# Performance work log

Hardware: AMD Instinct MI355X
Metric: run time of the kernel (lower is better)

Reference implementation:

```python
import jax, jax.numpy as jnp
import numpy as np

N = 50000      # nodes
E = 400000     # edges per hop
IN = 256       # in_channels
H = 4          # heads
C = 64         # out_channels per head
NEG = 0.2      # leaky relu negative slope


def setup_inputs() -> dict:
    key = jax.random.key(0)
    ks = jax.random.split(key, 10)
    x = jax.random.normal(ks[0], (N, IN), dtype=jnp.float32)
    edge_index1 = jax.random.randint(ks[1], (2, E), 0, N, dtype=jnp.int32)
    edge_index2 = jax.random.randint(ks[2], (2, E), 0, N, dtype=jnp.int32)
    s = 0.05
    Wl0 = jax.random.normal(ks[3], (IN, H * C), dtype=jnp.float32) * s
    Wr0 = jax.random.normal(ks[4], (IN, H * C), dtype=jnp.float32) * s
    att0 = jax.random.normal(ks[5], (H, C), dtype=jnp.float32) * s
    Wl1 = jax.random.normal(ks[6], (IN, H * C), dtype=jnp.float32) * s
    Wr1 = jax.random.normal(ks[7], (IN, H * C), dtype=jnp.float32) * s
    att1 = jax.random.normal(ks[8], (H, C), dtype=jnp.float32) * s
    return {"x": x, "Wl0": Wl0, "Wr0": Wr0, "att0": att0,
            "Wl1": Wl1, "Wr1": Wr1, "att1": att1,
            "edge_index1": edge_index1, "edge_index2": edge_index2}


def _gatv2_hop(x, Wl, Wr, att, src, dst):
    """One GATv2Conv hop (bias=False, residual=False, eval-mode dropout, concat=False)."""
    n = x.shape[0]
    xl = (x @ Wl).reshape(n, H, C)   # source-side projection
    xr = (x @ Wr).reshape(n, H, C)   # target-side projection
    # edge-wise GATv2 score: a^T leaky_relu(x_l[j] + x_r[i])
    m = jax.nn.leaky_relu(xl[src] + xr[dst], NEG)            # [E, H, C]
    e = jnp.einsum('ehc,hc->eh', m, att)                     # [E, H]
    # segment softmax over incoming edges of each destination node
    e_max = jax.lax.stop_gradient(
        jax.ops.segment_max(e, dst, num_segments=n))         # [N, H]
    ex = jnp.exp(e - e_max[dst])
    denom = jax.ops.segment_sum(ex, dst, num_segments=n)     # [N, H]
    alpha = ex / (denom[dst] + 1e-16)                        # [E, H]
    msg = xl[src] * alpha[:, :, None]                        # [E, H, C]
    out = jax.ops.segment_sum(msg, dst, num_segments=n)      # [N, H, C]
    return out.mean(axis=1)                                  # concat=False -> mean heads


def reference(x, Wl0, Wr0, att0, Wl1, Wr1, att1, edge_index1, edge_index2):
    n = x.shape[0]
    # hop 0: add_self_loops=True
    loop = jnp.arange(n, dtype=edge_index1.dtype)
    src0 = jnp.concatenate([edge_index1[0], loop])
    dst0 = jnp.concatenate([edge_index1[1], loop])
    out = _gatv2_hop(x, Wl0, Wr0, att0, src0, dst0)
    # hop 1: no self loops, scaled by 1/(k+1) = 1/2
    out = out + _gatv2_hop(x, Wl1, Wr1, att1, edge_index2[0], edge_index2[1]) / 2.0
    return out
```

## Files before the change

kernel.cpp:

```cpp
#include <hip/hip_runtime.h>

typedef unsigned int uint;
typedef unsigned short ushort;

typedef __bf16 bf16x8 __attribute__((ext_vector_type(8)));
typedef float f32x4 __attribute__((ext_vector_type(4)));
typedef float f32x2 __attribute__((ext_vector_type(2)));

#define CAP 48
#define RSTR 136

__device__ __forceinline__ ushort f2bf(float f) {
    uint u = __float_as_uint(f);
    u += 0x7fffu + ((u >> 16) & 1u);
    return (ushort)(u >> 16);
}
__device__ __forceinline__ void load_lds16(const ushort* g, ushort* l) {
    __builtin_amdgcn_global_load_lds(
        (const __attribute__((address_space(1))) void*)g,
        (__attribute__((address_space(3))) void*)l, 16, 0, 0);
}
__device__ __forceinline__ f32x2 up2(uint u) {
    f32x2 r;
    r.x = __uint_as_float(u << 16);
    r.y = __uint_as_float(u & 0xffff0000u);
    return r;
}

template<int CTRL>
__device__ __forceinline__ float dppadd(float p) {
    int t = __builtin_amdgcn_update_dpp(0, __float_as_int(p), CTRL, 0xf, 0xf, true);
    return p + __int_as_float(t);
}

__global__ __launch_bounds__(256) void prep_scatter(
    const float* __restrict__ X, ushort* __restrict__ Xb, int Nrows, int Mpad,
    const float* __restrict__ Wl0, const float* __restrict__ Wr0,
    const float* __restrict__ Wl1, const float* __restrict__ Wr1,
    ushort* __restrict__ Wt,
    const int* __restrict__ ei1, const int* __restrict__ ei2,
    int* __restrict__ cnt0, int* __restrict__ srcs0,
    int* __restrict__ cnt1, int* __restrict__ srcs1,
    int E1, int E2, int SB)
{
    int blk = blockIdx.x;
    if (blk < SB) {
        int e = blk * 256 + threadIdx.x;
        if (e < E1) {
            int d = ei1[E1 + e];
            int pos = atomicAdd(&cnt0[d], 1);
            if (pos < CAP) srcs0[(size_t)d * CAP + pos] = ei1[e];
        } else if (e < E1 + E2) {
            int e2 = e - E1;
            int d = ei2[E2 + e2];
            int pos = atomicAdd(&cnt1[d], 1);
            if (pos < CAP) srcs1[(size_t)d * CAP + pos] = ei2[e2];
        }
        return;
    }
    blk -= SB;
    const int BX = Mpad / 8;
    if (blk < BX) {
        int i = blk * 256 + threadIdx.x;
        int base = i * 8;
        int row = base >> 8;
        ushort o[8];
        if (row < Nrows) {
            float4 v0 = *(const float4*)(X + base);
            float4 v1 = *(const float4*)(X + base + 4);
            o[0] = f2bf(v0.x); o[1] = f2bf(v0.y); o[2] = f2bf(v0.z); o[3] = f2bf(v0.w);
            o[4] = f2bf(v1.x); o[5] = f2bf(v1.y); o[6] = f2bf(v1.z); o[7] = f2bf(v1.w);
        } else {
#pragma unroll
            for (int j = 0; j < 8; j++) o[j] = 0;
        }
        *(uint4*)(Xb + base) = *(const uint4*)o;
        return;
    }
    blk -= BX;
    int n = blk;
    int k = threadIdx.x;
    const float* W = (n < 256) ? Wl0 : (n < 512) ? Wr0 : (n < 768) ? Wl1 : Wr1;
    Wt[n * 256 + k] = f2bf(W[k * 256 + (n & 255)]);
}

__global__ __launch_bounds__(256, 2) void gemm_mfma(
    const ushort* __restrict__ Xb,
    const ushort* __restrict__ Wt,
    ushort* __restrict__ XP,
    int Nrows, int Pp, int nbshift)
{
    int b = blockIdx.x;
    int xcd = b & 7;
    int i = b >> 3;
    int p = xcd * Pp + (i >> nbshift);
    int j = i & ((1 << nbshift) - 1);
    const int m0 = p * 128;
    const int n0g = j * 128;

    __shared__ ushort SH[4 * 128 * 64];

    const int tid = threadIdx.x;
    const int w = tid >> 6, l = tid & 63;
    const int wm = w & 1, wn = w >> 1;

    f32x4 acc[4][4];
#pragma unroll
    for (int ii = 0; ii < 4; ii++)
#pragma unroll
        for (int jj = 0; jj < 4; jj++) acc[ii][jj] = (f32x4)(0.f);

    const int fr = l & 15, fq = l >> 4;
    int a_off[2][4], b_off[2][4];
#pragma unroll
    for (int g = 0; g < 2; g++)
#pragma unroll
        for (int t = 0; t < 4; t++) {
            int c = g * 4 + fq;
            int rA = wm * 64 + t * 16 + fr;
            a_off[g][t] = (rA * 8 + ((c + rA) & 7)) * 8;
            int rB = wn * 64 + t * 16 + fr;
            b_off[g][t] = (rB * 8 + ((c + rB) & 7)) * 8;
        }

    int srow[4], schunk[4];
#pragma unroll
    for (int rnd = 0; rnd < 4; rnd++) {
        int slot = rnd * 256 + tid;
        srow[rnd] = slot >> 3;
        schunk[rnd] = ((slot & 7) - srow[rnd]) & 7;
    }

#pragma unroll
    for (int rnd = 0; rnd < 4; rnd++) {
        load_lds16(Xb + (size_t)(m0 + srow[rnd]) * 256 + schunk[rnd] * 8,
                   &SH[(rnd * 256 + w * 64) * 8]);
        load_lds16(Wt + (size_t)(n0g + srow[rnd]) * 256 + schunk[rnd] * 8,
                   &SH[8192 + (rnd * 256 + w * 64) * 8]);
    }
    __syncthreads();

    int cur = 0;
    for (int t = 0; t < 4; t++) {
        const ushort* As = SH + cur * 16384;
        const ushort* Bs = As + 8192;
        if (t < 3) {
            ushort* An = SH + (cur ^ 1) * 16384;
            ushort* Bn = An + 8192;
            const int k0n = (t + 1) * 64;
#pragma unroll
            for (int rnd = 0; rnd < 4; rnd++) {
                load_lds16(Xb + (size_t)(m0 + srow[rnd]) * 256 + k0n + schunk[rnd] * 8,
                           &An[(rnd * 256 + w * 64) * 8]);
                load_lds16(Wt + (size_t)(n0g + srow[rnd]) * 256 + k0n + schunk[rnd] * 8,
                           &Bn[(rnd * 256 + w * 64) * 8]);
            }
        }
#pragma unroll
        for (int g = 0; g < 2; g++) {
            bf16x8 a[4], bfr[4];
#pragma unroll
            for (int t4 = 0; t4 < 4; t4++) {
                a[t4]   = *(const bf16x8*)(As + a_off[g][t4]);
                bfr[t4] = *(const bf16x8*)(Bs + b_off[g][t4]);
            }
#pragma unroll
            for (int mi = 0; mi < 4; mi++)
#pragma unroll
                for (int ni = 0; ni < 4; ni++)
                    acc[mi][ni] = __builtin_amdgcn_mfma_f32_16x16x32_bf16(
                        a[mi], bfr[ni], acc[mi][ni], 0, 0, 0);
        }
        __syncthreads();
        cur ^= 1;
    }

    ushort* OUT = XP + (size_t)(n0g >> 8) * ((size_t)Nrows * 256);
    const int colbase = n0g & 255;
    const int cb = wn * 64 + fr;
#pragma unroll
    for (int r = 0; r < 2; r++) {
        __syncthreads();
#pragma unroll
        for (int mm = 0; mm < 2; mm++) {
            int mi = 2 * r + mm;
            int brb = (wm * 32 + mm * 16 + fq * 4) * RSTR + cb;
#pragma unroll
            for (int reg = 0; reg < 4; reg++)
#pragma unroll
                for (int ni = 0; ni < 4; ni++)
                    SH[brb + reg * RSTR + ni * 16] = f2bf(acc[mi][ni][reg]);
        }
        __syncthreads();
        int br = tid >> 2;
        int grow = m0 + (br >> 5) * 64 + (2 * r + ((br >> 4) & 1)) * 16 + (br & 15);
        bool ok = (grow < Nrows);
        int cc = (tid & 3) * 8;
#pragma unroll
        for (int q = 0; q < 4; q++) {
            uint4 v = *(const uint4*)(SH + br * RSTR + cc + q * 32);
            if (ok) *(uint4*)(OUT + (size_t)grow * 256 + colbase + cc + q * 32) = v;
        }
    }
}

__device__ __forceinline__ uint4 pair_load(const ushort* __restrict__ XL, int sv,
                                           int e, int cp, uint hl, uint sub16)
{
    int eA = (e     < cp) ? e     : cp;
    int eB = (e + 1 < cp) ? e + 1 : cp;
    uint sA = (uint)__builtin_amdgcn_readlane(sv, eA) * 512u;
    uint sB = (uint)__builtin_amdgcn_readlane(sv, eB) * 512u;
    uint off = sA + hl * (sB - sA) + sub16;
    return *(const uint4*)((const char*)XL + off);
}

__device__ __forceinline__ void eaccp(uint4 raw, int deadB, uint hl,
    const f32x2* __restrict__ xr2, const f32x2* __restrict__ av2,
    f32x2* __restrict__ acc, float& den)
{
    f32x2 xv[4];
    xv[0] = up2(raw.x);
    xv[1] = up2(raw.y);
    xv[2] = up2(raw.z);
    xv[3] = up2(raw.w);
    f32x2 p2 = (f32x2)(0.f);
#pragma unroll
    for (int k = 0; k < 4; k++) {
        f32x2 t = xv[k] + xr2[k];
        f32x2 u = t * 0.2f;
        t = __builtin_elementwise_max(t, u);
        p2 += t * av2[k];
    }
    float p = p2.x + p2.y;
    p = dppadd<0xB1>(p);
    p = dppadd<0x4E>(p);
    p = dppadd<0x141>(p);
    float pe = __expf(p);
    if (deadB & (int)hl) pe = 0.f;
    den += pe;
#pragma unroll
    for (int k = 0; k < 4; k++) acc[k] += xv[k] * pe;
}

__device__ __forceinline__ void gat_hop_core(
    const ushort* __restrict__ XL, const float* __restrict__ att,
    int mt, int sv, uint4 xrr, uint hl, uint sub, uint sub16,
    f32x2* __restrict__ acc, float& den)
{
#pragma unroll
    for (int k = 0; k < 4; k++) acc[k] = (f32x2)(0.f);
    den = 0.f;
    if (mt <= 0) return;

    f32x2 xr2[4];
    xr2[0] = up2(xrr.x);
    xr2[1] = up2(xrr.y);
    xr2[2] = up2(xrr.z);
    xr2[3] = up2(xrr.w);
    float4 a0 = *(const float4*)(att + sub * 8);
    float4 a1 = *(const float4*)(att + sub * 8 + 4);
    f32x2 av2[4];
    av2[0].x = a0.x; av2[0].y = a0.y;
    av2[1].x = a0.z; av2[1].y = a0.w;
    av2[2].x = a1.x; av2[2].y = a1.y;
    av2[3].x = a1.z; av2[3].y = a1.w;

    const int cp = mt - 1;
    uint4 pf0 = pair_load(XL, sv, 0, cp, hl, sub16);
    uint4 pf1 = pair_load(XL, sv, 2, cp, hl, sub16);
    uint4 pf2 = pair_load(XL, sv, 4, cp, hl, sub16);
    for (int i = 0; i < mt; i += 6) {
        uint4 c0 = pf0, c1 = pf1, c2 = pf2;
        pf0 = pair_load(XL, sv, i + 6,  cp, hl, sub16);
        pf1 = pair_load(XL, sv, i + 8,  cp, hl, sub16);
        pf2 = pair_load(XL, sv, i + 10, cp, hl, sub16);
        eaccp(c0, (i + 1 >= mt) ? 1 : 0, hl, xr2, av2, acc, den);
        if (i + 2 < mt)
            eaccp(c1, (i + 3 >= mt) ? 1 : 0, hl, xr2, av2, acc, den);
        if (i + 4 < mt)
            eaccp(c2, (i + 5 >= mt) ? 1 : 0, hl, xr2, av2, acc, den);
    }
}

__global__ __launch_bounds__(256) void gat_fused(
    const ushort* __restrict__ XL0, const ushort* __restrict__ XR0,
    const float* __restrict__ att0,
    const int* __restrict__ cnt0, const int* __restrict__ srcs0,
    int self0, float scale0,
    const ushort* __restrict__ XL1, const ushort* __restrict__ XR1,
    const float* __restrict__ att1,
    const int* __restrict__ cnt1, const int* __restrict__ srcs1,
    float scale1,
    const float* __restrict__ base, float* __restrict__ outp, int N)
{
    int d = blockIdx.x * 4 + (threadIdx.x >> 6);
    if (d >= N) return;
    int lane = threadIdx.x & 63;
    uint hl = (uint)(lane >> 5);
    uint sub = (uint)(lane & 31);
    uint sub16 = sub * 16u;

    int idx0 = lane - self0;
    idx0 = idx0 < 0 ? 0 : (idx0 > CAP - 1 ? CAP - 1 : idx0);
    int sv0 = srcs0[(size_t)d * CAP + idx0];
    int m0 = __builtin_amdgcn_readfirstlane(cnt0[d]);
    uint4 xrr0 = *(const uint4*)((const char*)XR0 + (uint)d * 512u + sub16);

    int sv1 = 0, m1 = 0;
    uint4 xrr1 = {0, 0, 0, 0};
    if (cnt1) {
        int idx1 = lane > CAP - 1 ? CAP - 1 : lane;
        sv1 = srcs1[(size_t)d * CAP + idx1];
        m1 = __builtin_amdgcn_readfirstlane(cnt1[d]);
        xrr1 = *(const uint4*)((const char*)XR1 + (uint)d * 512u + sub16);
    }

    if (m0 > CAP) m0 = CAP;
    const int mt0 = m0 + self0;
    if (self0 && lane == 0) sv0 = d;
    if (m1 > CAP) m1 = CAP;

    f32x2 acc0[4];
    float den0;
    gat_hop_core(XL0, att0, mt0, sv0, xrr0, hl, sub, sub16, acc0, den0);

    float v[8];
    den0 += __shfl_xor(den0, 32);
    float s0 = scale0 / (den0 + 1e-16f);
    if (cnt1) {
        f32x2 acc1[4];
        float den1;
        gat_hop_core(XL1, att1, m1, sv1, xrr1, hl, sub, sub16, acc1, den1);
        den1 += __shfl_xor(den1, 32);
        float s1 = scale1 / (den1 + 1e-16f);
#pragma unroll
        for (int k = 0; k < 4; k++) {
            v[2 * k]     = acc0[k].x * s0 + acc1[k].x * s1;
            v[2 * k + 1] = acc0[k].y * s0 + acc1[k].y * s1;
        }
    } else {
#pragma unroll
        for (int k = 0; k < 4; k++) {
            v[2 * k]     = acc0[k].x * s0;
            v[2 * k + 1] = acc0[k].y * s0;
        }
    }
#pragma unroll
    for (int j = 0; j < 8; j++) {
        v[j] += __shfl_xor(v[j], 8);
        v[j] += __shfl_xor(v[j], 16);
        v[j] += __shfl_xor(v[j], 32);
    }
    if (lane < 8) {
        float* dst = outp + (size_t)d * 64 + lane * 8;
        float4 w0 = {v[0], v[1], v[2], v[3]};
        float4 w1 = {v[4], v[5], v[6], v[7]};
        if (base) {
            float4 b0 = *(const float4*)(base + (size_t)d * 64 + lane * 8);
            float4 b1 = *(const float4*)(base + (size_t)d * 64 + lane * 8 + 4);
            w0.x += b0.x; w0.y += b0.y; w0.z += b0.z; w0.w += b0.w;
            w1.x += b1.x; w1.y += b1.y; w1.z += b1.z; w1.w += b1.w;
        }
        *(float4*)dst = w0;
        *(float4*)(dst + 4) = w1;
    }
}

extern "C" void kernel_launch(void* const* d_in, const int* in_sizes, int n_in,
                              void* d_out, int out_size, void* d_ws, size_t ws_size,
                              hipStream_t stream)
{
    const float* x    = (const float*)d_in[0];
    const float* Wl0  = (const float*)d_in[1];
    const float* Wr0  = (const float*)d_in[2];
    const float* att0 = (const float*)d_in[3];
    const float* Wl1  = (const float*)d_in[4];
    const float* Wr1  = (const float*)d_in[5];
    const float* att1 = (const float*)d_in[6];
    const int* ei1 = (const int*)d_in[7];
    const int* ei2 = (const int*)d_in[8];

    const int N  = in_sizes[0] / 256;
    const int E1 = in_sizes[7] / 2;
    const int E2 = in_sizes[8] / 2;
    const int Mpad = ((N + 1023) / 1024) * 1024;
    const int P  = Mpad / 128;
    const int Pp = P / 8;
    const size_t NB = (size_t)N * 256;

    char* ws = (char*)d_ws;
    size_t off = 0;
    ushort* Xb  = (ushort*)(ws + off); off += (size_t)Mpad * 256 * sizeof(ushort);
    ushort* Wt  = (ushort*)(ws + off); off += (size_t)1024 * 256 * sizeof(ushort);
    int* cnt0   = (int*)(ws + off);    off += (size_t)N * sizeof(int);
    int* cnt1   = (int*)(ws + off);    off += (size_t)N * sizeof(int);
    int* srcs0  = (int*)(ws + off);    off += (size_t)N * CAP * sizeof(int);
    int* srcs1  = (int*)(ws + off);    off += (size_t)N * CAP * sizeof(int);
    ushort* XP  = (ushort*)(ws + off);
    size_t need_mega = off + 4 * NB * sizeof(ushort);
    const bool mega = (ws_size >= need_mega);
    float* outf = (float*)d_out;

    hipMemsetAsync(cnt0, 0, 2 * (size_t)N * sizeof(int), stream);

    const int BX = Mpad / 8;
    const int SB = (E1 + E2 + 255) / 256;
    prep_scatter<<<SB + BX + 1024, 256, 0, stream>>>(
        x, Xb, N, Mpad, Wl0, Wr0, Wl1, Wr1, Wt,
        ei1, ei2, cnt0, srcs0, cnt1, srcs1, E1, E2, SB);

    int aggblk = (N + 3) / 4;
    if (mega) {
        gemm_mfma<<<P * 8, 256, 0, stream>>>(Xb, Wt, XP, N, Pp, 3);
        gat_fused<<<aggblk, 256, 0, stream>>>(
            XP, XP + NB, att0, cnt0, srcs0, 1, 0.25f,
            XP + 2 * NB, XP + 3 * NB, att1, cnt1, srcs1, 0.125f,
            nullptr, outf, N);
    } else {
        gemm_mfma<<<P * 4, 256, 0, stream>>>(Xb, Wt, XP, N, Pp, 2);
        gat_fused<<<aggblk, 256, 0, stream>>>(
            XP, XP + NB, att0, cnt0, srcs0, 1, 0.25f,
            nullptr, nullptr, nullptr, nullptr, nullptr, 0.f,
            nullptr, outf, N);
        gemm_mfma<<<P * 4, 256, 0, stream>>>(Xb, Wt + 512 * 256, XP, N, Pp, 2);
        gat_fused<<<aggblk, 256, 0, stream>>>(
            XP, XP + NB, att1, cnt1, srcs1, 0, 0.125f,
            nullptr, nullptr, nullptr, nullptr, nullptr, 0.f,
            outf, outf, N);
    }
}
```

Before: 253.3 us.

## Issue all first-16-edge gathers for both hops upfront with inline asm loads

Replaces the per-hop software-pipelined gather loop with a single upfront burst of 16 global_load_dwordx4 per wave: 8 edge pairs for hop 0 and 8 for hop 1. Waits are placed with explicit vmcnt so hop-1 loads stay in flight while hop 0 is computed. Edges beyond 16 fall back to a simple serial loop. A launch_bounds occupancy hint of 4 is added. The aim is more memory-level parallelism on the random neighbor gathers, at the cost of many more live VGPRs. Edges past 16 lose prefetching.

```diff
diff --git a/kernel.cpp b/kernel.cpp
--- a/kernel.cpp
+++ b/kernel.cpp
@@ -6,6 +6,7 @@
 typedef __bf16 bf16x8 __attribute__((ext_vector_type(8)));
 typedef float f32x4 __attribute__((ext_vector_type(4)));
 typedef float f32x2 __attribute__((ext_vector_type(2)));
+typedef uint u32x4 __attribute__((ext_vector_type(4)));
 
 #define CAP 48
 #define RSTR 136
@@ -32,6 +33,10 @@
     int t = __builtin_amdgcn_update_dpp(0, __float_as_int(p), CTRL, 0xf, 0xf, true);
     return p + __int_as_float(t);
 }
+
+#define GLOAD(dst, voff, basep) \
+    asm volatile("global_load_dwordx4 %0, %1, %2" \
+                 : "=v"(dst) : "v"(voff), "s"(basep) : "memory")
 
 __global__ __launch_bounds__(256) void prep_scatter(
     const float* __restrict__ X, ushort* __restrict__ Xb, int Nrows, int Mpad,
@@ -204,26 +209,24 @@
     }
 }
 
-__device__ __forceinline__ uint4 pair_load(const ushort* __restrict__ XL, int sv,
-                                           int e, int cp, uint hl, uint sub16)
+__device__ __forceinline__ uint pair_voff(int sv, int e, int cp, uint hl, uint sub16)
 {
     int eA = (e     < cp) ? e     : cp;
     int eB = (e + 1 < cp) ? e + 1 : cp;
     uint sA = (uint)__builtin_amdgcn_readlane(sv, eA) * 512u;
     uint sB = (uint)__builtin_amdgcn_readlane(sv, eB) * 512u;
-    uint off = sA + hl * (sB - sA) + sub16;
-    return *(const uint4*)((const char*)XL + off);
-}
-
-__device__ __forceinline__ void eaccp(uint4 raw, int deadB, uint hl,
+    return (hl ? sB : sA) + sub16;
+}
+
+__device__ __forceinline__ void eaccp(u32x4 raw, int deadB, uint hl,
     const f32x2* __restrict__ xr2, const f32x2* __restrict__ av2,
     f32x2* __restrict__ acc, float& den)
 {
     f32x2 xv[4];
-    xv[0] = up2(raw.x);
-    xv[1] = up2(raw.y);
-    xv[2] = up2(raw.z);
-    xv[3] = up2(raw.w);
+    xv[0] = up2(raw[0]);
+    xv[1] = up2(raw[1]);
+    xv[2] = up2(raw[2]);
+    xv[3] = up2(raw[3]);
     f32x2 p2 = (f32x2)(0.f);
 #pragma unroll
     for (int k = 0; k < 4; k++) {
@@ -243,47 +246,7 @@
     for (int k = 0; k < 4; k++) acc[k] += xv[k] * pe;
 }
 
-__device__ __forceinline__ void gat_hop_core(
-    const ushort* __restrict__ XL, const float* __restrict__ att,
-    int mt, int sv, uint4 xrr, uint hl, uint sub, uint sub16,
-    f32x2* __restrict__ acc, float& den)
-{
-#pragma unroll
-    for (int k = 0; k < 4; k++) acc[k] = (f32x2)(0.f);
-    den = 0.f;
-    if (mt <= 0) return;
-
-    f32x2 xr2[4];
-    xr2[0] = up2(xrr.x);
-    xr2[1] = up2(xrr.y);
-    xr2[2] = up2(xrr.z);
-    xr2[3] = up2(xrr.w);
-    float4 a0 = *(const float4*)(att + sub * 8);
-    float4 a1 = *(const float4*)(att + sub * 8 + 4);
-    f32x2 av2[4];
-    av2[0].x = a0.x; av2[0].y = a0.y;
-    av2[1].x = a0.z; av2[1].y = a0.w;
-    av2[2].x = a1.x; av2[2].y = a1.y;
-    av2[3].x = a1.z; av2[3].y = a1.w;
-
-    const int cp = mt - 1;
-    uint4 pf0 = pair_load(XL, sv, 0, cp, hl, sub16);
-    uint4 pf1 = pair_load(XL, sv, 2, cp, hl, sub16);
-    uint4 pf2 = pair_load(XL, sv, 4, cp, hl, sub16);
-    for (int i = 0; i < mt; i += 6) {
-        uint4 c0 = pf0, c1 = pf1, c2 = pf2;
-        pf0 = pair_load(XL, sv, i + 6,  cp, hl, sub16);
-        pf1 = pair_load(XL, sv, i + 8,  cp, hl, sub16);
-        pf2 = pair_load(XL, sv, i + 10, cp, hl, sub16);
-        eaccp(c0, (i + 1 >= mt) ? 1 : 0, hl, xr2, av2, acc, den);
-        if (i + 2 < mt)
-            eaccp(c1, (i + 3 >= mt) ? 1 : 0, hl, xr2, av2, acc, den);
-        if (i + 4 < mt)
-            eaccp(c2, (i + 5 >= mt) ? 1 : 0, hl, xr2, av2, acc, den);
-    }
-}
-
-__global__ __launch_bounds__(256) void gat_fused(
+__global__ __launch_bounds__(256, 4) void gat_fused(
     const ushort* __restrict__ XL0, const ushort* __restrict__ XR0,
     const float* __restrict__ att0,
     const int* __restrict__ cnt0, const int* __restrict__ srcs0,
@@ -296,42 +259,110 @@
 {
     int d = blockIdx.x * 4 + (threadIdx.x >> 6);
     if (d >= N) return;
-    int lane = threadIdx.x & 63;
-    uint hl = (uint)(lane >> 5);
-    uint sub = (uint)(lane & 31);
-    uint sub16 = sub * 16u;
+    const int lane = threadIdx.x & 63;
+    const uint hl = (uint)(lane >> 5);
+    const uint sub = (uint)(lane & 31);
+    const uint sub16 = sub * 16u;
+    const bool two = (cnt1 != nullptr);
 
     int idx0 = lane - self0;
     idx0 = idx0 < 0 ? 0 : (idx0 > CAP - 1 ? CAP - 1 : idx0);
     int sv0 = srcs0[(size_t)d * CAP + idx0];
     int m0 = __builtin_amdgcn_readfirstlane(cnt0[d]);
-    uint4 xrr0 = *(const uint4*)((const char*)XR0 + (uint)d * 512u + sub16);
+    u32x4 xrr0 = *(const u32x4*)((const char*)XR0 + (uint)d * 512u + sub16);
+    float4 a00 = *(const float4*)(att0 + sub * 8);
+    float4 a01 = *(const float4*)(att0 + sub * 8 + 4);
 
     int sv1 = 0, m1 = 0;
-    uint4 xrr1 = {0, 0, 0, 0};
-    if (cnt1) {
+    u32x4 xrr1 = (u32x4)(0u);
+    float4 a10 = {0.f, 0.f, 0.f, 0.f}, a11 = {0.f, 0.f, 0.f, 0.f};
+    if (two) {
         int idx1 = lane > CAP - 1 ? CAP - 1 : lane;
         sv1 = srcs1[(size_t)d * CAP + idx1];
         m1 = __builtin_amdgcn_readfirstlane(cnt1[d]);
-        xrr1 = *(const uint4*)((const char*)XR1 + (uint)d * 512u + sub16);
+        xrr1 = *(const u32x4*)((const char*)XR1 + (uint)d * 512u + sub16);
+        a10 = *(const float4*)(att1 + sub * 8);
+        a11 = *(const float4*)(att1 + sub * 8 + 4);
     }
 
     if (m0 > CAP) m0 = CAP;
     const int mt0 = m0 + self0;
     if (self0 && lane == 0) sv0 = d;
+    if (mt0 == 0) sv0 = d;
     if (m1 > CAP) m1 = CAP;
+    const int mt1 = m1;
+    if (two && mt1 == 0) sv1 = d;
+
+    f32x2 xr20[4], av20[4], xr21[4], av21[4];
+    xr20[0] = up2(xrr0[0]); xr20[1] = up2(xrr0[1]);
+    xr20[2] = up2(xrr0[2]); xr20[3] = up2(xrr0[3]);
+    av20[0].x = a00.x; av20[0].y = a00.y;
+    av20[1].x = a00.z; av20[1].y = a00.w;
+    av20[2].x = a01.x; av20[2].y = a01.y;
+    av20[3].x = a01.z; av20[3].y = a01.w;
+    xr21[0] = up2(xrr1[0]); xr21[1] = up2(xrr1[1]);
+    xr21[2] = up2(xrr1[2]); xr21[3] = up2(xrr1[3]);
+    av21[0].x = a10.x; av21[0].y = a10.y;
+    av21[1].x = a10.z; av21[1].y = a10.w;
+    av21[2].x = a11.x; av21[2].y = a11.y;
+    av21[3].x = a11.z; av21[3].y = a11.w;
+
+    const int cp0 = mt0 > 0 ? mt0 - 1 : 0;
+    const int cp1 = mt1 > 0 ? mt1 - 1 : 0;
+    uint vo0[8], vo1[8];
+#pragma unroll
+    for (int k = 0; k < 8; k++) vo0[k] = pair_voff(sv0, 2 * k, cp0, hl, sub16);
+    if (two) {
+#pragma unroll
+        for (int k = 0; k < 8; k++) vo1[k] = pair_voff(sv1, 2 * k, cp1, hl, sub16);
+    }
+
+    __builtin_amdgcn_sched_barrier(0);
+    u32x4 p0[8], p1[8];
+#pragma unroll
+    for (int k = 0; k < 8; k++) GLOAD(p0[k], vo0[k], XL0);
+    if (two) {
+#pragma unroll
+        for (int k = 0; k < 8; k++) GLOAD(p1[k], vo1[k], XL1);
+        asm volatile("s_waitcnt vmcnt(8)" ::: "memory");
+    } else {
+        asm volatile("s_waitcnt vmcnt(0)" ::: "memory");
+    }
+    __builtin_amdgcn_sched_barrier(0);
 
     f32x2 acc0[4];
-    float den0;
-    gat_hop_core(XL0, att0, mt0, sv0, xrr0, hl, sub, sub16, acc0, den0);
-
-    float v[8];
+    float den0 = 0.f;
+#pragma unroll
+    for (int k = 0; k < 4; k++) acc0[k] = (f32x2)(0.f);
+#pragma unroll
+    for (int k = 0; k < 8; k++)
+        if (2 * k < mt0)
+            eaccp(p0[k], (2 * k + 1 >= mt0) ? 1 : 0, hl, xr20, av20, acc0, den0);
+    for (int i = 16; i < mt0; i += 2) {
+        uint vo = pair_voff(sv0, i, cp0, hl, sub16);
+        u32x4 c = *(const u32x4*)((const char*)XL0 + vo);
+        eaccp(c, (i + 1 >= mt0) ? 1 : 0, hl, xr20, av20, acc0, den0);
+    }
     den0 += __shfl_xor(den0, 32);
     float s0 = scale0 / (den0 + 1e-16f);
-    if (cnt1) {
+
+    float v[8];
+    if (two) {
+        asm volatile("s_waitcnt vmcnt(0)" ::: "memory");
+        __builtin_amdgcn_sched_barrier(0);
         f32x2 acc1[4];
-        float den1;
-        gat_hop_core(XL1, att1, m1, sv1, xrr1, hl, sub, sub16, acc1, den1);
+        float den1 = 0.f;
+#pragma unroll
+        for (int k = 0; k < 4; k++) acc1[k] = (f32x2)(0.f);
+#pragma unroll
+        for (int k = 0; k < 8; k++)
+            if (2 * k < mt1)
+                eaccp(p1[k], (2 * k + 1 >= mt1) ? 1 : 0, hl, xr21, av21, acc1, den1);
+        for (int i = 16; i < mt1; i += 2) {
+            uint vo = pair_voff(sv1, i, cp1, hl, sub16);
+            u32x4 c = *(const u32x4*)((const char*)XL1 + vo);
+            eaccp(c, (i + 1 >= mt1) ? 1 : 0, hl, xr21, av21, acc1, den1);
+        }
         den1 += __shfl_xor(den1, 32);
         float s1 = scale1 / (den1 + 1e-16f);
 #pragma unroll
```

After: 263.2 us. 3.9% more time.
